# Kernel optimization log

Measured on AMD Instinct MI355X. Metric: run time of the kernel, lower is better.

Reference implementation:

```python
import jax, jax.numpy as jnp
import numpy as np

NUM_HEADS = 16

def setup_inputs() -> dict:
    key = jax.random.key(0)
    ks = jax.random.split(key, 5)
    b, c, w, h = 2, 1024, 48, 48
    sc = 0.02
    return {
        "x": jax.random.normal(ks[0], (b, c, w, h), jnp.float32),
        "Wqkv": jax.random.normal(ks[1], (3 * c, c), jnp.float32) * sc,
        "bqkv": jax.random.normal(ks[2], (3 * c,), jnp.float32) * sc,
        "Wo": jax.random.normal(ks[3], (c, c), jnp.float32) * sc,
        "bo": jax.random.normal(ks[4], (c,), jnp.float32) * sc,
    }

def reference(x, Wqkv, bqkv, Wo, bo):
    b, c, w, h = x.shape
    n = NUM_HEADS
    hd = c // n
    s = w * h
    # [b,c,w,h] -> tokens [b, s, c]
    xs = x.transpose(0, 2, 3, 1).reshape(b, s, c)
    qkv = xs @ Wqkv.T + bqkv                       # [b, s, 3c]
    # rearrange 'b s (three n hd) -> three b n s hd'
    qkv = qkv.reshape(b, s, 3, n, hd).transpose(2, 0, 3, 1, 4)
    q, k, v = qkv[0], qkv[1], qkv[2]               # [b, n, s, hd]
    score = jnp.einsum('bnqh,bnkh->bnqk', q, k) / jnp.sqrt(jnp.float32(hd))
    # module uses a soft causal mask: subtract 10000 above the diagonal
    mask = 10000.0 * jnp.triu(jnp.ones((s, s), dtype=score.dtype), k=1)
    attn = jax.nn.softmax(score - mask, axis=-1)   # [b, n, s, s]
    z = jnp.einsum('bnqk,bnkh->bqnh', attn, v).reshape(b, s, c)
    out = z @ Wo.T + bo                            # [b, s, c]
    return out.reshape(b, w, h, c).transpose(0, 3, 1, 2)
```

## Files before the change

kernel.cpp:

```cpp
#include <hip/hip_runtime.h>

typedef __bf16 bf16;
typedef __bf16 bf16x8 __attribute__((ext_vector_type(8)));
typedef float floatx4 __attribute__((ext_vector_type(4)));

static constexpr int S = 2304;
static constexpr int C = 1024;
static constexpr int NHEAD = 16;
static constexpr int HDIM = 64;
static constexpr int BATCH = 2;
static constexpr float QSCALE = 0.18033688011112042f;
static constexpr int QSPLIT = 18;
static constexpr int NACC = S - QSPLIT * 64;

__global__ __launch_bounds__(256) void k_zero(float4* __restrict__ p, int n4) {
  int i = blockIdx.x * 256 + threadIdx.x;
  if (i < n4) p[i] = float4{0.f, 0.f, 0.f, 0.f};
}

__global__ __launch_bounds__(256) void k_convert(const float* __restrict__ src,
                                                 bf16* __restrict__ dst, int n8) {
  int i = blockIdx.x * 256 + threadIdx.x;
  if (i >= n8) return;
  float4 a = *(const float4*)(src + (size_t)i * 8);
  float4 b = *(const float4*)(src + (size_t)i * 8 + 4);
  bf16x8 o;
  o[0] = (bf16)a.x; o[1] = (bf16)a.y; o[2] = (bf16)a.z; o[3] = (bf16)a.w;
  o[4] = (bf16)b.x; o[5] = (bf16)b.y; o[6] = (bf16)b.z; o[7] = (bf16)b.w;
  *(bf16x8*)(dst + (size_t)i * 8) = o;
}

__global__ __launch_bounds__(256) void k_transpose(const float* __restrict__ x,
                                                   bf16* __restrict__ xs) {
  __shared__ bf16 T[64 * 72];
  int c0 = blockIdx.x * 64, t0 = blockIdx.y * 64, b = blockIdx.z;
  int tid = threadIdx.x;
  const float* xb = x + (size_t)b * C * S;
#pragma unroll
  for (int it = 0; it < 4; ++it) {
    int idx = it * 256 + tid;
    int rc = idx >> 4, t4 = idx & 15;
    float4 v = *(const float4*)(xb + (size_t)(c0 + rc) * S + t0 + t4 * 4);
    T[(t4 * 4 + 0) * 72 + rc] = (bf16)v.x;
    T[(t4 * 4 + 1) * 72 + rc] = (bf16)v.y;
    T[(t4 * 4 + 2) * 72 + rc] = (bf16)v.z;
    T[(t4 * 4 + 3) * 72 + rc] = (bf16)v.w;
  }
  __syncthreads();
  bf16* xsb = xs + (size_t)b * S * C;
#pragma unroll
  for (int it = 0; it < 2; ++it) {
    int idx = it * 256 + tid;
    int rt = idx >> 3, c8 = idx & 7;
    bf16x8 v;
#pragma unroll
    for (int i = 0; i < 8; ++i) v[i] = T[rt * 72 + c8 * 8 + i];
    *(bf16x8*)(xsb + (size_t)(t0 + rt) * C + c0 + c8 * 8) = v;
  }
}

__device__ __forceinline__ void g2l16(const bf16* g, bf16* l) {
  __builtin_amdgcn_global_load_lds(
      (const __attribute__((address_space(1))) void*)g,
      (__attribute__((address_space(3))) void*)l, 16, 0, 0);
}

template <int EPI>
__global__ __launch_bounds__(256) void k_gemm_bt(const bf16* __restrict__ A,
                                                 const bf16* __restrict__ Bt,
                                                 const float* __restrict__ bias,
                                                 bf16* __restrict__ q,
                                                 bf16* __restrict__ k,
                                                 bf16* __restrict__ v,
                                                 float* __restrict__ outf) {
  constexpr int K = C;
  __shared__ bf16 As[128 * 64];
  __shared__ bf16 Bs[128 * 64];
  int tid = threadIdx.x;
  int w = tid >> 6, lane = tid & 63, ln = lane & 15, quad = lane >> 4;
  int m0 = blockIdx.y * 128, n0 = blockIdx.x * 128;
  int moff = (w >> 1) * 64, noff = (w & 1) * 64;
  floatx4 acc[4][4] = {};

  int sr[4], sc[4];
#pragma unroll
  for (int it = 0; it < 4; ++it) {
    int L = (it * 4 + w) * 64 + lane;
    sr[it] = L >> 3;
    sc[it] = (L & 7) ^ (sr[it] & 7);
  }

  for (int k0 = 0; k0 < K; k0 += 64) {
    __syncthreads();
#pragma unroll
    for (int it = 0; it < 4; ++it) {
      int cb = (it * 4 + w) * 64;
      g2l16(A + (size_t)(m0 + sr[it]) * K + k0 + sc[it] * 8, As + cb * 8);
      g2l16(Bt + (size_t)(n0 + sr[it]) * K + k0 + sc[it] * 8, Bs + cb * 8);
    }
    __syncthreads();
#pragma unroll
    for (int t = 0; t < 2; ++t) {
      bf16x8 af[4], bfr[4];
#pragma unroll
      for (int i = 0; i < 4; ++i) {
        int ra = moff + i * 16 + ln;
        af[i]  = *(const bf16x8*)(As + ra * 64 + (((t * 4 + quad) ^ (ra & 7))) * 8);
        int rb = noff + i * 16 + ln;
        bfr[i] = *(const bf16x8*)(Bs + rb * 64 + (((t * 4 + quad) ^ (rb & 7))) * 8);
      }
#pragma unroll
      for (int im = 0; im < 4; ++im)
#pragma unroll
        for (int in = 0; in < 4; ++in)
          acc[im][in] = __builtin_amdgcn_mfma_f32_16x16x32_bf16(
              af[im], bfr[in], acc[im][in], 0, 0, 0);
    }
  }

  int bidx = (m0 >= S) ? 1 : 0;
  if (EPI == 0) {
#pragma unroll
    for (int in = 0; in < 4; ++in) {
      int j = n0 + noff + in * 16 + ln;
      float bv = bias[j];
      int three = j >> 10;
      int head = (j >> 6) & 15;
      int hdi = j & 63;
#pragma unroll
      for (int im = 0; im < 4; ++im) {
        int mbase = m0 + moff + im * 16 + quad * 4;
        int tb = mbase - bidx * S;
        if (three == 2) {
          union { ushort4 u; bf16 h[4]; } P;
#pragma unroll
          for (int r = 0; r < 4; ++r) P.h[r] = (bf16)(acc[im][in][r] + bv);
          *(ushort4*)(v + ((size_t)(bidx * NHEAD + head) * HDIM + hdi) * S + tb) = P.u;
        } else if (three == 0) {
          bf16* dst = q + ((size_t)(bidx * NHEAD + head) * S + tb) * HDIM + hdi;
#pragma unroll
          for (int r = 0; r < 4; ++r)
            dst[(size_t)r * HDIM] = (bf16)((acc[im][in][r] + bv) * QSCALE);
        } else {
          bf16* dst = k + ((size_t)(bidx * NHEAD + head) * S + tb) * HDIM + hdi;
#pragma unroll
          for (int r = 0; r < 4; ++r) dst[(size_t)r * HDIM] = (bf16)(acc[im][in][r] + bv);
        }
      }
    }
  } else {
#pragma unroll
    for (int in = 0; in < 4; ++in) {
      int co = n0 + noff + in * 16 + ln;
      float bv = bias[co];
#pragma unroll
      for (int im = 0; im < 4; ++im) {
        int mbase = m0 + moff + im * 16 + quad * 4;
        int tb = mbase - bidx * S;
        float4 st;
        st.x = acc[im][in][0] + bv;
        st.y = acc[im][in][1] + bv;
        st.z = acc[im][in][2] + bv;
        st.w = acc[im][in][3] + bv;
        *(float4*)(outf + ((size_t)bidx * C + co) * S + tb) = st;
      }
    }
  }
}

__global__ __launch_bounds__(256) void k_attn_part(const bf16* __restrict__ Qg,
                                                   const bf16* __restrict__ Kg,
                                                   const bf16* __restrict__ Vtg,
                                                   bf16* __restrict__ z,
                                                   float* __restrict__ Oacc,
                                                   float* __restrict__ Lacc) {
  __shared__ bf16 Ks[2][64 * 64];
  __shared__ bf16 Vs[2][64 * 64];
  __shared__ bf16 Pt[64 * 64];
  int i = blockIdx.x;
  int xcd = i & 7, j = i >> 3;
  int grp = j / 54, r = j % 54;
  int bh = xcd + 8 * grp;
  int qi, lo, hi;
  bool single = (r >= 36);
  if (!single) {
    qi = 35 - (r >> 1);
    int c = r & 1;
    lo = c * (qi + 1) / 2;
    hi = (c + 1) * (qi + 1) / 2;
  } else {
    qi = 53 - r;
    lo = 0;
    hi = qi + 1;
  }
  int b = bh >> 4, h = bh & 15;
  int tid = threadIdx.x;
  int w = tid >> 6, lane = tid & 63, ln = lane & 15, quad = lane >> 4;
  int q0 = qi * 64;
  int qg = q0 + w * 16 + ln;

  const bf16* kb = Kg + (size_t)bh * S * HDIM;
  const bf16* vb = Vtg + (size_t)bh * HDIM * S;

  int s_row = tid >> 3, s_c8 = tid & 7;
  int s_cs = s_c8 ^ (s_row & 7);
  int s_row2 = s_row + 32;
  int s_cs2 = s_c8 ^ (s_row2 & 7);
  size_t kOff1 = (size_t)s_row * HDIM + s_cs * 8;
  size_t kOff2 = (size_t)s_row2 * HDIM + s_cs2 * 8;
  size_t vOff1 = (size_t)s_row * S + s_cs * 8;
  size_t vOff2 = (size_t)s_row2 * S + s_cs2 * 8;

  const bf16* qb = Qg + ((size_t)bh * S + qg) * HDIM + quad * 8;
  bf16x8 qf0 = *(const bf16x8*)qb;
  bf16x8 qf1 = *(const bf16x8*)(qb + 32);

  float lsum = 0.f;
  floatx4 o_acc[4] = {};

  int prow = w * 16 + ln;
  int psw = ln & 7;
  bf16* ptw = Pt + prow * 64 + (quad & 1) * 4;
  const bf16* ptr = Pt + prow * 64;

  const bf16* kb0 = kb + (size_t)lo * 64 * HDIM;
  const bf16* vb0 = vb + (size_t)lo * 64;
  g2l16(kb0 + kOff1, Ks[0] + tid * 8);
  g2l16(vb0 + vOff1, Vs[0] + tid * 8);
  g2l16(kb0 + kOff2, Ks[0] + (256 + tid) * 8);
  g2l16(vb0 + vOff2, Vs[0] + (256 + tid) * 8);

  const bf16* kbn = kb0 + (size_t)64 * HDIM;
  const bf16* vbn = vb0 + 64;

#pragma unroll 1
  for (int kt = lo; kt < hi; ++kt) {
    int cur = (kt - lo) & 1;
    __syncthreads();

    if (kt + 1 < hi) {
      bf16* kd = Ks[1 - cur];
      bf16* vd = Vs[1 - cur];
      g2l16(kbn + kOff1, kd + tid * 8);
      g2l16(vbn + vOff1, vd + tid * 8);
      g2l16(kbn + kOff2, kd + (256 + tid) * 8);
      g2l16(vbn + vOff2, vd + (256 + tid) * 8);
      kbn += (size_t)64 * HDIM;
      vbn += 64;
    }

    floatx4 s_acc[4] = {};
#pragma unroll
    for (int kf = 0; kf < 4; ++kf) {
      int row = kf * 16 + ln;
      int sw = row & 7;
      bf16x8 k0 = *(const bf16x8*)(Ks[cur] + row * 64 + (sw ^ quad) * 8);
      bf16x8 k1 = *(const bf16x8*)(Ks[cur] + row * 64 + ((4 ^ sw) ^ quad) * 8);
      s_acc[kf] = __builtin_amdgcn_mfma_f32_16x16x32_bf16(k0, qf0, s_acc[kf], 0, 0, 0);
      s_acc[kf] = __builtin_amdgcn_mfma_f32_16x16x32_bf16(k1, qf1, s_acc[kf], 0, 0, 0);
    }

    if (kt < qi) {
#pragma unroll
      for (int kf = 0; kf < 4; ++kf) {
        union { ushort4 u; bf16 hh[4]; } P;
#pragma unroll
        for (int rr = 0; rr < 4; ++rr) {
          float pv = exp2f(s_acc[kf][rr]);
          lsum += pv;
          P.hh[rr] = (bf16)pv;
        }
        *(ushort4*)(ptw + (((kf * 2 + (quad >> 1)) ^ psw)) * 8) = P.u;
      }
    } else {
#pragma unroll
      for (int kf = 0; kf < 4; ++kf) {
        union { ushort4 u; bf16 hh[4]; } P;
#pragma unroll
        for (int rr = 0; rr < 4; ++rr) {
          int kl = kf * 16 + quad * 4 + rr;
          float pv = (kl > w * 16 + ln) ? 0.f : exp2f(s_acc[kf][rr]);
          lsum += pv;
          P.hh[rr] = (bf16)pv;
        }
        *(ushort4*)(ptw + (((kf * 2 + (quad >> 1)) ^ psw)) * 8) = P.u;
      }
    }

#pragma unroll
    for (int t = 0; t < 2; ++t) {
      bf16x8 pf = *(const bf16x8*)(ptr + (((t * 4 + quad) ^ psw)) * 8);
#pragma unroll
      for (int hf = 0; hf < 4; ++hf) {
        int row = hf * 16 + ln;
        int sw = row & 7;
        bf16x8 vf = *(const bf16x8*)(Vs[cur] + row * 64 + (((t * 4 + quad) ^ sw)) * 8);
        o_acc[hf] = __builtin_amdgcn_mfma_f32_16x16x32_bf16(vf, pf, o_acc[hf], 0, 0, 0);
      }
    }
  }

  lsum += __shfl_xor(lsum, 16);
  lsum += __shfl_xor(lsum, 32);

  if (single) {
    float inv = 1.f / lsum;
    bf16* dst = z + ((size_t)b * S + qg) * C + h * HDIM + quad * 4;
#pragma unroll
    for (int hf = 0; hf < 4; ++hf) {
      union { ushort4 u; bf16 hh[4]; } P;
#pragma unroll
      for (int rr = 0; rr < 4; ++rr) P.hh[rr] = (bf16)(o_acc[hf][rr] * inv);
      *(ushort4*)(dst + hf * 16) = P.u;
    }
  } else {
    int qa = qg - QSPLIT * 64;
    if (lane < 16) atomicAdd(&Lacc[bh * NACC + qa], lsum);
#pragma unroll
    for (int hf = 0; hf < 4; ++hf)
#pragma unroll
      for (int rr = 0; rr < 4; ++rr)
        atomicAdd(&Oacc[((size_t)bh * 64 + hf * 16 + quad * 4 + rr) * NACC + qa],
                  o_acc[hf][rr]);
  }
}

__global__ __launch_bounds__(256) void k_norm(const float* __restrict__ Oacc,
                                              const float* __restrict__ Lacc,
                                              bf16* __restrict__ z) {
  __shared__ float T[64 * 65];
  int qt = blockIdx.x, bh = blockIdx.y;
  int b = bh >> 4, h = bh & 15;
  int qrel0 = qt * 64;
  int q0 = QSPLIT * 64 + qrel0;
  int tid = threadIdx.x;
  int q4 = (tid & 15) * 4, hd0 = tid >> 4;
  float4 lv = *(const float4*)(Lacc + bh * NACC + qrel0 + q4);
  float inv0 = 1.f / lv.x, inv1 = 1.f / lv.y, inv2 = 1.f / lv.z, inv3 = 1.f / lv.w;
#pragma unroll
  for (int hf = 0; hf < 4; ++hf) {
    int hd = hf * 16 + hd0;
    float4 v = *(const float4*)(Oacc + ((size_t)bh * 64 + hd) * NACC + qrel0 + q4);
    T[(q4 + 0) * 65 + hd] = v.x * inv0;
    T[(q4 + 1) * 65 + hd] = v.y * inv1;
    T[(q4 + 2) * 65 + hd] = v.z * inv2;
    T[(q4 + 3) * 65 + hd] = v.w * inv3;
  }
  __syncthreads();
#pragma unroll
  for (int it = 0; it < 2; ++it) {
    int idx = it * 256 + tid;
    int qq = idx >> 3, c8 = idx & 7;
    bf16x8 o;
#pragma unroll
    for (int k = 0; k < 8; ++k) o[k] = (bf16)T[qq * 65 + c8 * 8 + k];
    *(bf16x8*)(z + ((size_t)b * S + q0 + qq) * C + h * HDIM + c8 * 8) = o;
  }
}

extern "C" void kernel_launch(void* const* d_in, const int* in_sizes, int n_in,
                              void* d_out, int out_size, void* d_ws, size_t ws_size,
                              hipStream_t stream) {
  const float* x    = (const float*)d_in[0];
  const float* Wqkv = (const float*)d_in[1];
  const float* bqkv = (const float*)d_in[2];
  const float* Wo   = (const float*)d_in[3];
  const float* bo   = (const float*)d_in[4];
  float* out = (float*)d_out;

  bf16* ws = (bf16*)d_ws;
  const size_t tok = (size_t)BATCH * S * C;
  bf16* xs   = ws;
  bf16* Qg   = ws + tok;
  bf16* Kg   = ws + 2 * tok;
  bf16* Vtg  = ws + 3 * tok;
  bf16* Wqb  = ws + 4 * tok;
  bf16* Wob  = Wqb + (size_t)3 * C * C;
  float* Oacc = (float*)(Wob + (size_t)C * C);
  float* Lacc = Oacc + (size_t)32 * 64 * NACC;
  bf16* z    = xs;

  k_zero<<<2340, 256, 0, stream>>>((float4*)Oacc, 599040);
  k_convert<<<(3 * C * C / 8 + 255) / 256, 256, 0, stream>>>(Wqkv, Wqb, 3 * C * C / 8);
  k_convert<<<(C * C / 8 + 255) / 256, 256, 0, stream>>>(Wo, Wob, C * C / 8);
  k_transpose<<<dim3(C / 64, S / 64, BATCH), 256, 0, stream>>>(x, xs);
  k_gemm_bt<0><<<dim3(3 * C / 128, BATCH * S / 128), 256, 0, stream>>>(
      xs, Wqb, bqkv, Qg, Kg, Vtg, nullptr);
  k_attn_part<<<dim3(1728), 256, 0, stream>>>(Qg, Kg, Vtg, z, Oacc, Lacc);
  k_norm<<<dim3(18, 32), 256, 0, stream>>>(Oacc, Lacc, z);
  k_gemm_bt<1><<<dim3(C / 128, BATCH * S / 128), 256, 0, stream>>>(
      z, Wob, bo, nullptr, nullptr, nullptr, out);
}
```

Baseline: 219.1 us.

## Process 128 query rows per attention block with eight waves sharing K/V tiles

The attention kernel now uses 512-thread blocks covering 128 query rows instead of 64. Each staged 64-key K/V tile is reused by twice as many queries, which halves K/V global-to-LDS traffic and the number of blocks. The split-K scheduling is re-indexed for 128-row query tiles. Waves whose queries lie before the last key tile skip its compute, which leaves some waves idle on the diagonal tile. Larger blocks also raise LDS use and may lower occupancy.

```diff
diff --git a/kernel.cpp b/kernel.cpp
--- a/kernel.cpp
+++ b/kernel.cpp
@@ -168,7 +168,7 @@
   }
 }
 
-__global__ __launch_bounds__(256) void k_attn_part(const bf16* __restrict__ Qg,
+__global__ __launch_bounds__(512) void k_attn_part(const bf16* __restrict__ Qg,
                                                    const bf16* __restrict__ Kg,
                                                    const bf16* __restrict__ Vtg,
                                                    bf16* __restrict__ z,
@@ -176,40 +176,37 @@
                                                    float* __restrict__ Lacc) {
   __shared__ bf16 Ks[2][64 * 64];
   __shared__ bf16 Vs[2][64 * 64];
-  __shared__ bf16 Pt[64 * 64];
+  __shared__ bf16 Pt[128 * 64];
   int i = blockIdx.x;
   int xcd = i & 7, j = i >> 3;
-  int grp = j / 54, r = j % 54;
+  int grp = j / 27, r = j % 27;
   int bh = xcd + 8 * grp;
   int qi, lo, hi;
-  bool single = (r >= 36);
+  bool single = (r >= 18);
   if (!single) {
-    qi = 35 - (r >> 1);
-    int c = r & 1;
-    lo = c * (qi + 1) / 2;
-    hi = (c + 1) * (qi + 1) / 2;
+    qi = 17 - (r >> 1);
+    lo = (r & 1) * (qi + 1);
+    hi = lo + qi + 1;
   } else {
-    qi = 53 - r;
+    qi = 26 - r;
     lo = 0;
-    hi = qi + 1;
+    hi = 2 * qi + 2;
   }
   int b = bh >> 4, h = bh & 15;
   int tid = threadIdx.x;
   int w = tid >> 6, lane = tid & 63, ln = lane & 15, quad = lane >> 4;
-  int q0 = qi * 64;
-  int qg = q0 + w * 16 + ln;
+  int q0 = qi * 128;
+  int qw = q0 + w * 16;
+  int qg = qw + ln;
+  int ktd = qw >> 6;
 
   const bf16* kb = Kg + (size_t)bh * S * HDIM;
   const bf16* vb = Vtg + (size_t)bh * HDIM * S;
 
   int s_row = tid >> 3, s_c8 = tid & 7;
   int s_cs = s_c8 ^ (s_row & 7);
-  int s_row2 = s_row + 32;
-  int s_cs2 = s_c8 ^ (s_row2 & 7);
-  size_t kOff1 = (size_t)s_row * HDIM + s_cs * 8;
-  size_t kOff2 = (size_t)s_row2 * HDIM + s_cs2 * 8;
-  size_t vOff1 = (size_t)s_row * S + s_cs * 8;
-  size_t vOff2 = (size_t)s_row2 * S + s_cs2 * 8;
+  size_t kOff = (size_t)s_row * HDIM + s_cs * 8;
+  size_t vOff = (size_t)s_row * S + s_cs * 8;
 
   const bf16* qb = Qg + ((size_t)bh * S + qg) * HDIM + quad * 8;
   bf16x8 qf0 = *(const bf16x8*)qb;
@@ -222,13 +219,12 @@
   int psw = ln & 7;
   bf16* ptw = Pt + prow * 64 + (quad & 1) * 4;
   const bf16* ptr = Pt + prow * 64;
+  int qloc = (w & 3) * 16 + ln;
 
   const bf16* kb0 = kb + (size_t)lo * 64 * HDIM;
   const bf16* vb0 = vb + (size_t)lo * 64;
-  g2l16(kb0 + kOff1, Ks[0] + tid * 8);
-  g2l16(vb0 + vOff1, Vs[0] + tid * 8);
-  g2l16(kb0 + kOff2, Ks[0] + (256 + tid) * 8);
-  g2l16(vb0 + vOff2, Vs[0] + (256 + tid) * 8);
+  g2l16(kb0 + kOff, Ks[0] + tid * 8);
+  g2l16(vb0 + vOff, Vs[0] + tid * 8);
 
   const bf16* kbn = kb0 + (size_t)64 * HDIM;
   const bf16* vbn = vb0 + 64;
@@ -239,15 +235,13 @@
     __syncthreads();
 
     if (kt + 1 < hi) {
-      bf16* kd = Ks[1 - cur];
-      bf16* vd = Vs[1 - cur];
-      g2l16(kbn + kOff1, kd + tid * 8);
-      g2l16(vbn + vOff1, vd + tid * 8);
-      g2l16(kbn + kOff2, kd + (256 + tid) * 8);
-      g2l16(vbn + vOff2, vd + (256 + tid) * 8);
+      g2l16(kbn + kOff, Ks[1 - cur] + tid * 8);
+      g2l16(vbn + vOff, Vs[1 - cur] + tid * 8);
       kbn += (size_t)64 * HDIM;
       vbn += 64;
     }
+
+    if (kt > ktd) continue;
 
     floatx4 s_acc[4] = {};
 #pragma unroll
@@ -260,7 +254,7 @@
       s_acc[kf] = __builtin_amdgcn_mfma_f32_16x16x32_bf16(k1, qf1, s_acc[kf], 0, 0, 0);
     }
 
-    if (kt < qi) {
+    if (kt < ktd) {
 #pragma unroll
       for (int kf = 0; kf < 4; ++kf) {
         union { ushort4 u; bf16 hh[4]; } P;
@@ -279,7 +273,7 @@
 #pragma unroll
         for (int rr = 0; rr < 4; ++rr) {
           int kl = kf * 16 + quad * 4 + rr;
-          float pv = (kl > w * 16 + ln) ? 0.f : exp2f(s_acc[kf][rr]);
+          float pv = (kl > qloc) ? 0.f : exp2f(s_acc[kf][rr]);
           lsum += pv;
           P.hh[rr] = (bf16)pv;
         }
@@ -386,7 +380,7 @@
   k_transpose<<<dim3(C / 64, S / 64, BATCH), 256, 0, stream>>>(x, xs);
   k_gemm_bt<0><<<dim3(3 * C / 128, BATCH * S / 128), 256, 0, stream>>>(
       xs, Wqb, bqkv, Qg, Kg, Vtg, nullptr);
-  k_attn_part<<<dim3(1728), 256, 0, stream>>>(Qg, Kg, Vtg, z, Oacc, Lacc);
+  k_attn_part<<<dim3(864), 512, 0, stream>>>(Qg, Kg, Vtg, z, Oacc, Lacc);
   k_norm<<<dim3(18, 32), 256, 0, stream>>>(Oacc, Lacc, z);
   k_gemm_bt<1><<<dim3(C / 128, BATCH * S / 128), 256, 0, stream>>>(
       z, Wob, bo, nullptr, nullptr, nullptr, out);
```

New measurement: 216.4 us. Within noise of the previous version (-1.2%).
